# Optimization experiments

Hardware: AMD Instinct MI355X
Metric: run time of the kernel (lower is better)

## Reference

```python
import jax, jax.numpy as jnp
import numpy as np

N_NODES = 100000
N_EDGES = 1600000
IN_F = 256
OUT_F = 64
ALPHA = 0.2  # LeakyReLU negative slope


def setup_inputs() -> dict:
    key = jax.random.key(0)
    k1, k2, k3, k4 = jax.random.split(key, 4)
    x = jax.random.normal(k1, (N_NODES, IN_F), dtype=jnp.float32)
    indices = jax.random.randint(k2, (2, N_EDGES), 0, N_NODES, dtype=jnp.int64)
    # xavier_uniform with gain=1.414 ~ U(-b, b), b = gain*sqrt(6/(fan_in+fan_out))
    bW = 1.414 * np.sqrt(6.0 / (IN_F + OUT_F))
    W = jax.random.uniform(k3, (IN_F, OUT_F), dtype=jnp.float32, minval=-bW, maxval=bW)
    ba = 1.414 * np.sqrt(6.0 / (2 * OUT_F + 1))
    a = jax.random.uniform(k4, (2 * OUT_F, 1), dtype=jnp.float32, minval=-ba, maxval=ba)
    return {"x": x, "indices": indices, "W": W, "a": a}


def reference(x, indices, W, a):
    # h = X @ W  -> [N, F_out]
    h = x @ W
    N = h.shape[0]
    src = indices[0]  # segment ids (softmax rows / aggregation targets)
    dst = indices[1]  # gathered neighbor features

    # e_ij = leakyrelu([h_i || h_j] @ a) = leakyrelu(h_i@a1 + h_j@a2)
    # (identical math to concatenation, avoids materializing [E, 2F])
    a1 = a[:OUT_F, 0]
    a2 = a[OUT_F:, 0]
    s1 = h @ a1  # [N]
    s2 = h @ a2  # [N]
    logits = s1[src] + s2[dst]  # [E]
    e = jnp.where(logits > 0, logits, ALPHA * logits)

    # segment softmax over edges grouped by src (sp_softmax)
    m = jax.ops.segment_max(e, src, num_segments=N)
    ex = jnp.exp(e - m[src])
    denom = jax.ops.segment_sum(ex, src, num_segments=N)
    att = ex / denom[src]  # [E]

    # h_prime[i] = sum_j att_ij * h_j  (sp_matmul: weighted scatter-aggregate)
    h_prime = jax.ops.segment_sum(att[:, None] * h[dst], src, num_segments=N)

    # concat=True -> ELU
    return jax.nn.elu(h_prime)
```

## Files before the change

kernel.cpp:

```cpp
#include <hip/hip_runtime.h>
#include <hip/hip_bf16.h>
#include <math.h>

#define NN 100000
#define NE 1600000
#define INF_ 256
#define OF 64

#define NPB 128
#define NB  782
#define CAPB 2560
#define ED (CAPB + 128)
#define GEMMB 782
#define P1B 512
#define CH1 ((NE + P1B - 1) / P1B)
#define OVCAP 8192

constexpr float LRELU_ALPHA = 0.2f;

typedef __attribute__((ext_vector_type(8))) short short8;
typedef __attribute__((ext_vector_type(4))) float f32x4;

static __device__ __forceinline__ unsigned short f2bf(float f) {
    union { float f; unsigned int u; } v; v.f = f;
    unsigned int r = v.u + 0x7fff + ((v.u >> 16) & 1);
    return (unsigned short)(r >> 16);
}
static __device__ __forceinline__ float bf2f(unsigned short b) {
    union { unsigned int u; float f; } v; v.u = ((unsigned int)b) << 16;
    return v.f;
}
static __device__ __forceinline__ unsigned int pkbf(float a, float b) {
    union { __hip_bfloat162 h; unsigned int u; } c;
    c.h = __float22bfloat162_rn(make_float2(a, b));
    return c.u;
}

union S8 { short8 s; unsigned int u[4]; };

__global__ __launch_bounds__(256) void k_fused1(const float* __restrict__ x,
                                                const float* __restrict__ W,
                                                const float* __restrict__ a,
                                                const int* __restrict__ idx,
                                                int* __restrict__ cur_b,
                                                int* __restrict__ pairs,
                                                int2* __restrict__ ov_list,
                                                unsigned short* __restrict__ h,
                                                float* __restrict__ s1,
                                                float* __restrict__ s2) {
    __shared__ __align__(16) char smem[43008];
    int tid = threadIdx.x;

    if (blockIdx.x < GEMMB) {
        short* Wf  = (short*)smem;
        float* wal = (float*)(smem + 40960);

        {
            float t1 = 0.f, t2 = 0.f;
            const float* wr = W + tid * OF;
#pragma unroll 8
            for (int c = 0; c < OF; ++c) {
                float w = wr[c];
                t1 += w * a[c];
                t2 += w * a[OF + c];
            }
            wal[tid] = t1;
            wal[256 + tid] = t2;
        }
        __syncthreads();

        for (int i = tid; i < 2560; i += 256) {
            int ks = i / 320;
            int rem = i - ks * 320;
            int ct = rem >> 6;
            int l  = rem & 63;
            int kb = ks * 32 + ((l >> 4) << 3);
            int c  = l & 15;
            S8 v;
            if (ct < 4) {
                int col = ct * 16 + c;
#pragma unroll
                for (int j = 0; j < 4; ++j)
                    v.u[j] = pkbf(W[(size_t)(kb + 2 * j) * OF + col],
                                  W[(size_t)(kb + 2 * j + 1) * OF + col]);
            } else if (c < 2) {
                const float* src = wal + c * 256;
#pragma unroll
                for (int j = 0; j < 4; ++j)
                    v.u[j] = pkbf(src[kb + 2 * j], src[kb + 2 * j + 1]);
            } else {
#pragma unroll
                for (int j = 0; j < 4; ++j) v.u[j] = 0u;
            }
            ((short8*)Wf)[i] = v.s;
        }
        __syncthreads();

        int wid = tid >> 6, lane = tid & 63;
        int rowbase = blockIdx.x * 128 + wid * 32;
        int r0 = rowbase + (lane & 15);
        int koff = (lane >> 4) << 3;

        f32x4 acc[2][5];
#pragma unroll
        for (int rt = 0; rt < 2; ++rt)
#pragma unroll
            for (int ct = 0; ct < 5; ++ct) acc[rt][ct] = (f32x4){0.f, 0.f, 0.f, 0.f};

#pragma unroll 1
        for (int ks = 0; ks < 8; ++ks) {
            S8 af[2];
#pragma unroll
            for (int rt = 0; rt < 2; ++rt) {
                int r = r0 + rt * 16;
                if (r < NN) {
                    const float* p = x + (size_t)r * INF_ + ks * 32 + koff;
                    float4 xa = *(const float4*)p;
                    float4 xb = *(const float4*)(p + 4);
                    af[rt].u[0] = pkbf(xa.x, xa.y);
                    af[rt].u[1] = pkbf(xa.z, xa.w);
                    af[rt].u[2] = pkbf(xb.x, xb.y);
                    af[rt].u[3] = pkbf(xb.z, xb.w);
                } else {
#pragma unroll
                    for (int j = 0; j < 4; ++j) af[rt].u[j] = 0u;
                }
            }
#pragma unroll
            for (int rt = 0; rt < 2; ++rt)
#pragma unroll
                for (int ct = 0; ct < 5; ++ct)
                    acc[rt][ct] = __builtin_amdgcn_mfma_f32_16x16x32_bf16(
                        af[rt].s, ((short8*)Wf)[(ks * 5 + ct) * 64 + lane], acc[rt][ct], 0, 0, 0);
        }

        int c = lane & 15, rowq = lane >> 4;
#pragma unroll
        for (int rt = 0; rt < 2; ++rt) {
#pragma unroll
            for (int reg = 0; reg < 4; ++reg) {
                int r = rowbase + rt * 16 + rowq * 4 + reg;
                if (r < NN) {
#pragma unroll
                    for (int ct = 0; ct < 4; ++ct)
                        h[(size_t)r * OF + ct * 16 + c] = f2bf(acc[rt][ct][reg]);
                    float sv = acc[rt][4][reg];
                    if (c == 0)      s1[r] = sv;
                    else if (c == 1) s2[r] = sv;
                }
            }
        }
    } else {
        int blk = blockIdx.x - GEMMB;
        int* hist  = (int*)smem;
        int* gbase = (int*)smem + NB;
        for (int i = tid; i < NB; i += 256) hist[i] = 0;
        __syncthreads();
        int e0 = blk * CH1, e1 = min(e0 + CH1, NE);
        for (int e = e0 + tid; e < e1; e += 256)
            atomicAdd(&hist[idx[e] >> 7], 1);
        __syncthreads();
        for (int i = tid; i < NB; i += 256) {
            int c = hist[i];
            gbase[i] = c ? atomicAdd(&cur_b[i], c) : 0;
            hist[i] = 0;
        }
        __syncthreads();
        for (int e = e0 + tid; e < e1; e += 256) {
            int s = idx[e], d = idx[NE + e];
            int b = s >> 7;
            int p = gbase[b] + atomicAdd(&hist[b], 1);
            if (p < CAPB) pairs[b * CAPB + p] = ((s & 127) << 17) | d;
            else {
                int j = atomicAdd(&cur_b[NB], 1);
                if (j < OVCAP) ov_list[j] = make_int2(s, d);
            }
        }
    }
}

__global__ __launch_bounds__(256) void k_part2(const int* __restrict__ pairs,
                                               const int* __restrict__ cur_b,
                                               const int2* __restrict__ ov_list,
                                               const float* __restrict__ s1,
                                               const float* __restrict__ s2,
                                               int* __restrict__ start,
                                               int* __restrict__ deg,
                                               int2* __restrict__ el_g) {
    __shared__ int stage[ED];
    __shared__ int cnt[NPB], pfx[NPB], cur[NPB];
    __shared__ float s1l[NPB];
    __shared__ int extra;
    int tid = threadIdx.x, b = blockIdx.x;
    int node0 = b * NPB;

    if (tid < NPB) {
        cnt[tid] = 0;
        int g = node0 + tid;
        s1l[tid] = (g < NN) ? s1[g] : 0.f;
    }
    if (tid == 0) extra = 0;
    __syncthreads();

    int t_b = cur_b[b];
    int nin = min(t_b, CAPB);
    for (int i = tid; i < nin; i += 256) {
        int v = pairs[b * CAPB + i];
        stage[i] = v;
        atomicAdd(&cnt[v >> 17], 1);
    }
    if (t_b > CAPB) {
        int ovn = min(cur_b[NB], OVCAP);
        for (int i = tid; i < ovn; i += 256) {
            int2 e = ov_list[i];
            if ((e.x >> 7) == b) {
                int k = atomicAdd(&extra, 1);
                if (k < 128) {
                    stage[CAPB + k] = ((e.x & 127) << 17) | e.y;
                    atomicAdd(&cnt[e.x & 127], 1);
                }
            }
        }
    }
    __syncthreads();
    int ntot = nin + min(extra, 128);

    if (tid < NPB) pfx[tid] = cnt[tid];
    __syncthreads();
    for (int off = 1; off < NPB; off <<= 1) {
        int xv = (tid >= off && tid < NPB) ? pfx[tid - off] : 0;
        __syncthreads();
        if (tid < NPB) pfx[tid] += xv;
        __syncthreads();
    }
    if (tid < NPB) {
        int ex = pfx[tid] - cnt[tid];
        int g = node0 + tid;
        if (g < NN) { start[g] = b * CAPB + ex; deg[g] = cnt[tid]; }
        cur[tid] = ex;
    }
    __syncthreads();
    for (int i = tid; i < ntot; i += 256) {
        int v = stage[i];
        int ls = v >> 17, dst = v & 0x1FFFF;
        int p = atomicAdd(&cur[ls], 1);
        float lg = s1l[ls] + s2[dst];
        float elr = lg > 0.f ? lg : LRELU_ALPHA * lg;
        el_g[b * CAPB + p] = make_int2(dst, __float_as_int(expf(elr)));
    }
}

__global__ __launch_bounds__(256) void k_agg(const int2* __restrict__ el_g,
                                             const int* __restrict__ start,
                                             const int* __restrict__ deg,
                                             const unsigned short* __restrict__ h,
                                             float* __restrict__ out) {
    __shared__ int2 tile[4][64];
    int tid = threadIdx.x;
    int wid = tid >> 6, lane = tid & 63;
    int node = blockIdx.x * 4 + wid;
    if (node >= NN) return;

    int st = start[node];
    int dg = deg[node];
    int half = lane >> 5, f2 = lane & 31;
    float den = 0.f, ax = 0.f, ay = 0.f;

    for (int base = 0; base < dg; base += 64) {
        int cnt = min(64, dg - base);
        if (lane < cnt) {
            int2 pr = el_g[st + base + lane];
            den += __int_as_float(pr.y);
            tile[wid][lane] = pr;
        }
        asm volatile("s_waitcnt lgkmcnt(0)" ::: "memory");
#pragma unroll 4
        for (int j = half; j < cnt; j += 2) {
            int2 e = tile[wid][j];
            float ex = __int_as_float(e.y);
            unsigned int hv = *(const unsigned int*)(h + (size_t)e.x * OF + f2 * 2);
            ax += ex * bf2f((unsigned short)(hv & 0xFFFFu));
            ay += ex * bf2f((unsigned short)(hv >> 16));
        }
        asm volatile("" ::: "memory");
    }

#pragma unroll
    for (int off = 1; off < 64; off <<= 1) den += __shfl_xor(den, off, 64);
    ax += __shfl_xor(ax, 32, 64);
    ay += __shfl_xor(ay, 32, 64);

    float inv = den > 0.f ? 1.f / den : 0.f;
    float vx = ax * inv, vy = ay * inv;
    vx = vx > 0.f ? vx : expf(vx) - 1.f;
    vy = vy > 0.f ? vy : expf(vy) - 1.f;
    if (half == 0)
        *(float2*)(out + (size_t)node * OF + f2 * 2) = make_float2(vx, vy);
}

extern "C" void kernel_launch(void* const* d_in, const int* in_sizes, int n_in,
                              void* d_out, int out_size, void* d_ws, size_t ws_size,
                              hipStream_t stream) {
    const float* x   = (const float*)d_in[0];
    const int*   idx = (const int*)d_in[1];
    const float* W   = (const float*)d_in[2];
    const float* a   = (const float*)d_in[3];
    float* out = (float*)d_out;

    char* ws = (char*)d_ws;
    unsigned short* h = (unsigned short*)ws;  ws += sizeof(unsigned short) * (size_t)NN * OF;
    int*  pairs       = (int*)ws;             ws += sizeof(int) * (size_t)NB * CAPB;
    int2* el_g        = (int2*)ws;            ws += sizeof(int2) * (size_t)NB * CAPB;
    float* s1         = (float*)ws;           ws += sizeof(float) * NN;
    float* s2         = (float*)ws;           ws += sizeof(float) * NN;
    int*   start      = (int*)ws;             ws += sizeof(int) * NN;
    int*   deg        = (int*)ws;             ws += sizeof(int) * NN;
    int*   cur_b      = (int*)ws;             ws += sizeof(int) * (NB + 16);
    int2*  ov_list    = (int2*)ws;            ws += sizeof(int2) * OVCAP;

    hipMemsetAsync(cur_b, 0, sizeof(int) * (NB + 16), stream);
    k_fused1<<<GEMMB + P1B, 256, 0, stream>>>(x, W, a, idx, cur_b, pairs, ov_list, h, s1, s2);
    k_part2<<<NB, 256, 0, stream>>>(pairs, cur_b, ov_list, s1, s2, start, deg, el_g);
    k_agg<<<(NN + 3) / 4, 256, 0, stream>>>(el_g, start, deg, h, out);
}
```

Measured before the change: 289.0 us.

## Split fused GEMM/partition kernel and prefetch next x tile in GEMM

Breaks the fused kernel into three launches. A one-block prep kernel computes W@a once instead of in every GEMM block. A dedicated GEMM kernel with occupancy hint 4 register-prefetches the next K-slice of x while MFMAs run on the current one. The edge partition runs as its own kernel. This removes per-block redundant W@a work and hides x load latency, but gives up the overlap between GEMM and partition blocks and adds launch overhead.

```diff
diff --git a/kernel.cpp b/kernel.cpp
--- a/kernel.cpp
+++ b/kernel.cpp
@@ -38,143 +38,146 @@
 
 union S8 { short8 s; unsigned int u[4]; };
 
-__global__ __launch_bounds__(256) void k_fused1(const float* __restrict__ x,
-                                                const float* __restrict__ W,
-                                                const float* __restrict__ a,
-                                                const int* __restrict__ idx,
-                                                int* __restrict__ cur_b,
-                                                int* __restrict__ pairs,
-                                                int2* __restrict__ ov_list,
-                                                unsigned short* __restrict__ h,
-                                                float* __restrict__ s1,
-                                                float* __restrict__ s2) {
-    __shared__ __align__(16) char smem[43008];
+__global__ __launch_bounds__(256) void k_prep(const float* __restrict__ W,
+                                              const float* __restrict__ a,
+                                              float* __restrict__ wa) {
+    int r = threadIdx.x;
+    float t1 = 0.f, t2 = 0.f;
+#pragma unroll 8
+    for (int c = 0; c < OF; ++c) {
+        float w = W[r * OF + c];
+        t1 += w * a[c];
+        t2 += w * a[OF + c];
+    }
+    wa[r] = t1;
+    wa[256 + r] = t2;
+}
+
+__global__ __launch_bounds__(256, 4) void k_gemm(const float* __restrict__ x,
+                                                 const float* __restrict__ W,
+                                                 const float* __restrict__ wa,
+                                                 unsigned short* __restrict__ h,
+                                                 float* __restrict__ s1,
+                                                 float* __restrict__ s2) {
+    __shared__ short Wf[2560 * 8];
     int tid = threadIdx.x;
-
-    if (blockIdx.x < GEMMB) {
-        short* Wf  = (short*)smem;
-        float* wal = (float*)(smem + 40960);
-
-        {
-            float t1 = 0.f, t2 = 0.f;
-            const float* wr = W + tid * OF;
-#pragma unroll 8
-            for (int c = 0; c < OF; ++c) {
-                float w = wr[c];
-                t1 += w * a[c];
-                t2 += w * a[OF + c];
+    for (int i = tid; i < 2560; i += 256) {
+        int ks = i / 320;
+        int rem = i - ks * 320;
+        int ct = rem >> 6;
+        int l  = rem & 63;
+        int kb = ks * 32 + ((l >> 4) << 3);
+        int c  = l & 15;
+        S8 v;
+        if (ct < 4) {
+            int col = ct * 16 + c;
+#pragma unroll
+            for (int j = 0; j < 4; ++j)
+                v.u[j] = pkbf(W[(size_t)(kb + 2 * j) * OF + col],
+                              W[(size_t)(kb + 2 * j + 1) * OF + col]);
+        } else if (c < 2) {
+            const float* src = wa + c * 256;
+#pragma unroll
+            for (int j = 0; j < 4; ++j)
+                v.u[j] = pkbf(src[kb + 2 * j], src[kb + 2 * j + 1]);
+        } else {
+#pragma unroll
+            for (int j = 0; j < 4; ++j) v.u[j] = 0u;
+        }
+        ((short8*)Wf)[i] = v.s;
+    }
+    __syncthreads();
+
+    int wid = tid >> 6, lane = tid & 63;
+    int rowbase = blockIdx.x * 128 + wid * 32;
+    int r0 = rowbase + (lane & 15);
+    int koff = (lane >> 4) << 3;
+    bool ok0 = (r0 < NN), ok1 = (r0 + 16 < NN);
+    const float* p0 = x + (size_t)r0 * INF_ + koff;
+    const float* p1 = p0 + (size_t)16 * INF_;
+
+    f32x4 acc[2][5];
+#pragma unroll
+    for (int rt = 0; rt < 2; ++rt)
+#pragma unroll
+        for (int ct = 0; ct < 5; ++ct) acc[rt][ct] = (f32x4){0.f, 0.f, 0.f, 0.f};
+
+    float4 ca0, cb0, ca1, cb1;
+    float4 na0, nb0, na1, nb1;
+    ca0 = ok0 ? *(const float4*)p0 : make_float4(0, 0, 0, 0);
+    cb0 = ok0 ? *(const float4*)(p0 + 4) : make_float4(0, 0, 0, 0);
+    ca1 = ok1 ? *(const float4*)p1 : make_float4(0, 0, 0, 0);
+    cb1 = ok1 ? *(const float4*)(p1 + 4) : make_float4(0, 0, 0, 0);
+
+#pragma unroll 1
+    for (int ks = 0; ks < 8; ++ks) {
+        if (ks < 7) {
+            const float* q0 = p0 + (ks + 1) * 32;
+            const float* q1 = p1 + (ks + 1) * 32;
+            na0 = ok0 ? *(const float4*)q0 : make_float4(0, 0, 0, 0);
+            nb0 = ok0 ? *(const float4*)(q0 + 4) : make_float4(0, 0, 0, 0);
+            na1 = ok1 ? *(const float4*)q1 : make_float4(0, 0, 0, 0);
+            nb1 = ok1 ? *(const float4*)(q1 + 4) : make_float4(0, 0, 0, 0);
+        }
+        S8 af[2];
+        af[0].u[0] = pkbf(ca0.x, ca0.y); af[0].u[1] = pkbf(ca0.z, ca0.w);
+        af[0].u[2] = pkbf(cb0.x, cb0.y); af[0].u[3] = pkbf(cb0.z, cb0.w);
+        af[1].u[0] = pkbf(ca1.x, ca1.y); af[1].u[1] = pkbf(ca1.z, ca1.w);
+        af[1].u[2] = pkbf(cb1.x, cb1.y); af[1].u[3] = pkbf(cb1.z, cb1.w);
+#pragma unroll
+        for (int rt = 0; rt < 2; ++rt)
+#pragma unroll
+            for (int ct = 0; ct < 5; ++ct)
+                acc[rt][ct] = __builtin_amdgcn_mfma_f32_16x16x32_bf16(
+                    af[rt].s, ((short8*)Wf)[(ks * 5 + ct) * 64 + lane], acc[rt][ct], 0, 0, 0);
+        ca0 = na0; cb0 = nb0; ca1 = na1; cb1 = nb1;
+    }
+
+    int c = lane & 15, rowq = lane >> 4;
+#pragma unroll
+    for (int rt = 0; rt < 2; ++rt) {
+#pragma unroll
+        for (int reg = 0; reg < 4; ++reg) {
+            int r = rowbase + rt * 16 + rowq * 4 + reg;
+            if (r < NN) {
+#pragma unroll
+                for (int ct = 0; ct < 4; ++ct)
+                    h[(size_t)r * OF + ct * 16 + c] = f2bf(acc[rt][ct][reg]);
+                float sv = acc[rt][4][reg];
+                if (c == 0)      s1[r] = sv;
+                else if (c == 1) s2[r] = sv;
             }
-            wal[tid] = t1;
-            wal[256 + tid] = t2;
-        }
-        __syncthreads();
-
-        for (int i = tid; i < 2560; i += 256) {
-            int ks = i / 320;
-            int rem = i - ks * 320;
-            int ct = rem >> 6;
-            int l  = rem & 63;
-            int kb = ks * 32 + ((l >> 4) << 3);
-            int c  = l & 15;
-            S8 v;
-            if (ct < 4) {
-                int col = ct * 16 + c;
-#pragma unroll
-                for (int j = 0; j < 4; ++j)
-                    v.u[j] = pkbf(W[(size_t)(kb + 2 * j) * OF + col],
-                                  W[(size_t)(kb + 2 * j + 1) * OF + col]);
-            } else if (c < 2) {
-                const float* src = wal + c * 256;
-#pragma unroll
-                for (int j = 0; j < 4; ++j)
-                    v.u[j] = pkbf(src[kb + 2 * j], src[kb + 2 * j + 1]);
-            } else {
-#pragma unroll
-                for (int j = 0; j < 4; ++j) v.u[j] = 0u;
-            }
-            ((short8*)Wf)[i] = v.s;
-        }
-        __syncthreads();
-
-        int wid = tid >> 6, lane = tid & 63;
-        int rowbase = blockIdx.x * 128 + wid * 32;
-        int r0 = rowbase + (lane & 15);
-        int koff = (lane >> 4) << 3;
-
-        f32x4 acc[2][5];
-#pragma unroll
-        for (int rt = 0; rt < 2; ++rt)
-#pragma unroll
-            for (int ct = 0; ct < 5; ++ct) acc[rt][ct] = (f32x4){0.f, 0.f, 0.f, 0.f};
-
-#pragma unroll 1
-        for (int ks = 0; ks < 8; ++ks) {
-            S8 af[2];
-#pragma unroll
-            for (int rt = 0; rt < 2; ++rt) {
-                int r = r0 + rt * 16;
-                if (r < NN) {
-                    const float* p = x + (size_t)r * INF_ + ks * 32 + koff;
-                    float4 xa = *(const float4*)p;
-                    float4 xb = *(const float4*)(p + 4);
-                    af[rt].u[0] = pkbf(xa.x, xa.y);
-                    af[rt].u[1] = pkbf(xa.z, xa.w);
-                    af[rt].u[2] = pkbf(xb.x, xb.y);
-                    af[rt].u[3] = pkbf(xb.z, xb.w);
-                } else {
-#pragma unroll
-                    for (int j = 0; j < 4; ++j) af[rt].u[j] = 0u;
-                }
-            }
-#pragma unroll
-            for (int rt = 0; rt < 2; ++rt)
-#pragma unroll
-                for (int ct = 0; ct < 5; ++ct)
-                    acc[rt][ct] = __builtin_amdgcn_mfma_f32_16x16x32_bf16(
-                        af[rt].s, ((short8*)Wf)[(ks * 5 + ct) * 64 + lane], acc[rt][ct], 0, 0, 0);
-        }
-
-        int c = lane & 15, rowq = lane >> 4;
-#pragma unroll
-        for (int rt = 0; rt < 2; ++rt) {
-#pragma unroll
-            for (int reg = 0; reg < 4; ++reg) {
-                int r = rowbase + rt * 16 + rowq * 4 + reg;
-                if (r < NN) {
-#pragma unroll
-                    for (int ct = 0; ct < 4; ++ct)
-                        h[(size_t)r * OF + ct * 16 + c] = f2bf(acc[rt][ct][reg]);
-                    float sv = acc[rt][4][reg];
-                    if (c == 0)      s1[r] = sv;
-                    else if (c == 1) s2[r] = sv;
-                }
-            }
-        }
-    } else {
-        int blk = blockIdx.x - GEMMB;
-        int* hist  = (int*)smem;
-        int* gbase = (int*)smem + NB;
-        for (int i = tid; i < NB; i += 256) hist[i] = 0;
-        __syncthreads();
-        int e0 = blk * CH1, e1 = min(e0 + CH1, NE);
-        for (int e = e0 + tid; e < e1; e += 256)
-            atomicAdd(&hist[idx[e] >> 7], 1);
-        __syncthreads();
-        for (int i = tid; i < NB; i += 256) {
-            int c = hist[i];
-            gbase[i] = c ? atomicAdd(&cur_b[i], c) : 0;
-            hist[i] = 0;
-        }
-        __syncthreads();
-        for (int e = e0 + tid; e < e1; e += 256) {
-            int s = idx[e], d = idx[NE + e];
-            int b = s >> 7;
-            int p = gbase[b] + atomicAdd(&hist[b], 1);
-            if (p < CAPB) pairs[b * CAPB + p] = ((s & 127) << 17) | d;
-            else {
-                int j = atomicAdd(&cur_b[NB], 1);
-                if (j < OVCAP) ov_list[j] = make_int2(s, d);
-            }
+        }
+    }
+}
+
+__global__ __launch_bounds__(256) void k_part1(const int* __restrict__ idx,
+                                               int* __restrict__ cur_b,
+                                               int* __restrict__ pairs,
+                                               int2* __restrict__ ov_list) {
+    __shared__ int hist[NB];
+    __shared__ int gbase[NB];
+    int tid = threadIdx.x, blk = blockIdx.x;
+    for (int i = tid; i < NB; i += 256) hist[i] = 0;
+    __syncthreads();
+    int e0 = blk * CH1, e1 = min(e0 + CH1, NE);
+    for (int e = e0 + tid; e < e1; e += 256)
+        atomicAdd(&hist[idx[e] >> 7], 1);
+    __syncthreads();
+    for (int i = tid; i < NB; i += 256) {
+        int c = hist[i];
+        gbase[i] = c ? atomicAdd(&cur_b[i], c) : 0;
+        hist[i] = 0;
+    }
+    __syncthreads();
+    for (int e = e0 + tid; e < e1; e += 256) {
+        int s = idx[e], d = idx[NE + e];
+        int b = s >> 7;
+        int p = gbase[b] + atomicAdd(&hist[b], 1);
+        if (p < CAPB) pairs[b * CAPB + p] = ((s & 127) << 17) | d;
+        else {
+            int j = atomicAdd(&cur_b[NB], 1);
+            if (j < OVCAP) ov_list[j] = make_int2(s, d);
         }
     }
 }
@@ -317,9 +320,12 @@
     int*   deg        = (int*)ws;             ws += sizeof(int) * NN;
     int*   cur_b      = (int*)ws;             ws += sizeof(int) * (NB + 16);
     int2*  ov_list    = (int2*)ws;            ws += sizeof(int2) * OVCAP;
+    float* wa         = (float*)ws;           ws += sizeof(float) * 512;
 
     hipMemsetAsync(cur_b, 0, sizeof(int) * (NB + 16), stream);
-    k_fused1<<<GEMMB + P1B, 256, 0, stream>>>(x, W, a, idx, cur_b, pairs, ov_list, h, s1, s2);
+    k_prep<<<1, 256, 0, stream>>>(W, a, wa);
+    k_gemm<<<GEMMB, 256, 0, stream>>>(x, W, wa, h, s1, s2);
+    k_part1<<<P1B, 256, 0, stream>>>(idx, cur_b, pairs, ov_list);
     k_part2<<<NB, 256, 0, stream>>>(pairs, cur_b, ov_list, s1, s2, start, deg, el_g);
     k_agg<<<(NN + 3) / 4, 256, 0, stream>>>(el_g, start, deg, h, out);
 }
```

Result: slower. 296.3 us (+2.5%).

## Hoist W·a precompute into prep kernel and keep score fragment in registers

Applied to the files above, without the earlier changes.

Moves the per-block W·a reduction into a tiny separate kernel, so each GEMM block no longer recomputes it. The fifth MFMA column tile (attention scores) is held in per-lane registers instead of shared memory, which cuts LDS from 43 KB to 32 KB and adds launch bounds of 3 blocks per CU. The K loop is fully unrolled, and the row-bounds branches are replaced with clamped addresses so x loads can issue early. In exchange it adds an extra kernel launch and more register pressure, which could collide with the occupancy target.

```diff
diff --git a/kernel.cpp b/kernel.cpp
--- a/kernel.cpp
+++ b/kernel.cpp
@@ -38,103 +38,109 @@
 
 union S8 { short8 s; unsigned int u[4]; };
 
-__global__ __launch_bounds__(256) void k_fused1(const float* __restrict__ x,
-                                                const float* __restrict__ W,
-                                                const float* __restrict__ a,
-                                                const int* __restrict__ idx,
-                                                int* __restrict__ cur_b,
-                                                int* __restrict__ pairs,
-                                                int2* __restrict__ ov_list,
-                                                unsigned short* __restrict__ h,
-                                                float* __restrict__ s1,
-                                                float* __restrict__ s2) {
-    __shared__ __align__(16) char smem[43008];
+__global__ __launch_bounds__(256) void k_prep(const float* __restrict__ W,
+                                              const float* __restrict__ a,
+                                              float* __restrict__ wa) {
+    int r = threadIdx.x;
+    float t1 = 0.f, t2 = 0.f;
+#pragma unroll 8
+    for (int c = 0; c < OF; ++c) {
+        float w = W[r * OF + c];
+        t1 += w * a[c];
+        t2 += w * a[OF + c];
+    }
+    wa[r] = t1;
+    wa[256 + r] = t2;
+}
+
+__global__ __launch_bounds__(256, 3) void k_fused1(const float* __restrict__ x,
+                                                   const float* __restrict__ W,
+                                                   const float* __restrict__ wa,
+                                                   const int* __restrict__ idx,
+                                                   int* __restrict__ cur_b,
+                                                   int* __restrict__ pairs,
+                                                   int2* __restrict__ ov_list,
+                                                   unsigned short* __restrict__ h,
+                                                   float* __restrict__ s1,
+                                                   float* __restrict__ s2) {
+    __shared__ __align__(16) char smem[32768];
     int tid = threadIdx.x;
 
     if (blockIdx.x < GEMMB) {
-        short* Wf  = (short*)smem;
-        float* wal = (float*)(smem + 40960);
-
-        {
-            float t1 = 0.f, t2 = 0.f;
-            const float* wr = W + tid * OF;
-#pragma unroll 8
-            for (int c = 0; c < OF; ++c) {
-                float w = wr[c];
-                t1 += w * a[c];
-                t2 += w * a[OF + c];
-            }
-            wal[tid] = t1;
-            wal[256 + tid] = t2;
-        }
-        __syncthreads();
-
-        for (int i = tid; i < 2560; i += 256) {
-            int ks = i / 320;
-            int rem = i - ks * 320;
-            int ct = rem >> 6;
-            int l  = rem & 63;
+        short* Wf = (short*)smem;
+        for (int i = tid; i < 2048; i += 256) {
+            int ks = i >> 8;
+            int ct = (i >> 6) & 3;
+            int l  = i & 63;
             int kb = ks * 32 + ((l >> 4) << 3);
-            int c  = l & 15;
+            int col = ct * 16 + (l & 15);
             S8 v;
-            if (ct < 4) {
-                int col = ct * 16 + c;
-#pragma unroll
-                for (int j = 0; j < 4; ++j)
-                    v.u[j] = pkbf(W[(size_t)(kb + 2 * j) * OF + col],
-                                  W[(size_t)(kb + 2 * j + 1) * OF + col]);
-            } else if (c < 2) {
-                const float* src = wal + c * 256;
-#pragma unroll
-                for (int j = 0; j < 4; ++j)
-                    v.u[j] = pkbf(src[kb + 2 * j], src[kb + 2 * j + 1]);
-            } else {
-#pragma unroll
-                for (int j = 0; j < 4; ++j) v.u[j] = 0u;
-            }
+#pragma unroll
+            for (int j = 0; j < 4; ++j)
+                v.u[j] = pkbf(W[(size_t)(kb + 2 * j) * OF + col],
+                              W[(size_t)(kb + 2 * j + 1) * OF + col]);
             ((short8*)Wf)[i] = v.s;
         }
-        __syncthreads();
 
         int wid = tid >> 6, lane = tid & 63;
         int rowbase = blockIdx.x * 128 + wid * 32;
-        int r0 = rowbase + (lane & 15);
+        int c = lane & 15;
         int koff = (lane >> 4) << 3;
 
+        short8 frag5[8];
+        {
+#pragma unroll
+            for (int ks = 0; ks < 8; ++ks) {
+                S8 v;
+                if (c < 2) {
+                    const float* src = wa + c * 256 + ks * 32 + koff;
+                    float4 u0 = *(const float4*)src;
+                    float4 u1 = *(const float4*)(src + 4);
+                    v.u[0] = pkbf(u0.x, u0.y); v.u[1] = pkbf(u0.z, u0.w);
+                    v.u[2] = pkbf(u1.x, u1.y); v.u[3] = pkbf(u1.z, u1.w);
+                } else {
+                    v.u[0] = 0u; v.u[1] = 0u; v.u[2] = 0u; v.u[3] = 0u;
+                }
+                frag5[ks] = v.s;
+            }
+        }
+        __syncthreads();
+
+        int r0 = rowbase + c;
+        int rc0 = min(r0, NN - 1);
+        int rc1 = min(r0 + 16, NN - 1);
+        const float* p0 = x + (size_t)rc0 * INF_ + koff;
+        const float* p1 = x + (size_t)rc1 * INF_ + koff;
+
         f32x4 acc[2][5];
 #pragma unroll
         for (int rt = 0; rt < 2; ++rt)
 #pragma unroll
             for (int ct = 0; ct < 5; ++ct) acc[rt][ct] = (f32x4){0.f, 0.f, 0.f, 0.f};
 
-#pragma unroll 1
+#pragma unroll
         for (int ks = 0; ks < 8; ++ks) {
+            float4 xa0 = *(const float4*)(p0 + ks * 32);
+            float4 xb0 = *(const float4*)(p0 + ks * 32 + 4);
+            float4 xa1 = *(const float4*)(p1 + ks * 32);
+            float4 xb1 = *(const float4*)(p1 + ks * 32 + 4);
             S8 af[2];
+            af[0].u[0] = pkbf(xa0.x, xa0.y); af[0].u[1] = pkbf(xa0.z, xa0.w);
+            af[0].u[2] = pkbf(xb0.x, xb0.y); af[0].u[3] = pkbf(xb0.z, xb0.w);
+            af[1].u[0] = pkbf(xa1.x, xa1.y); af[1].u[1] = pkbf(xa1.z, xa1.w);
+            af[1].u[2] = pkbf(xb1.x, xb1.y); af[1].u[3] = pkbf(xb1.z, xb1.w);
 #pragma unroll
             for (int rt = 0; rt < 2; ++rt) {
-                int r = r0 + rt * 16;
-                if (r < NN) {
-                    const float* p = x + (size_t)r * INF_ + ks * 32 + koff;
-                    float4 xa = *(const float4*)p;
-                    float4 xb = *(const float4*)(p + 4);
-                    af[rt].u[0] = pkbf(xa.x, xa.y);
-                    af[rt].u[1] = pkbf(xa.z, xa.w);
-                    af[rt].u[2] = pkbf(xb.x, xb.y);
-                    af[rt].u[3] = pkbf(xb.z, xb.w);
-                } else {
-#pragma unroll
-                    for (int j = 0; j < 4; ++j) af[rt].u[j] = 0u;
-                }
-            }
-#pragma unroll
-            for (int rt = 0; rt < 2; ++rt)
-#pragma unroll
-                for (int ct = 0; ct < 5; ++ct)
+#pragma unroll
+                for (int ct = 0; ct < 4; ++ct)
                     acc[rt][ct] = __builtin_amdgcn_mfma_f32_16x16x32_bf16(
-                        af[rt].s, ((short8*)Wf)[(ks * 5 + ct) * 64 + lane], acc[rt][ct], 0, 0, 0);
-        }
-
-        int c = lane & 15, rowq = lane >> 4;
+                        af[rt].s, ((short8*)Wf)[(ks * 4 + ct) * 64 + lane], acc[rt][ct], 0, 0, 0);
+                acc[rt][4] = __builtin_amdgcn_mfma_f32_16x16x32_bf16(
+                    af[rt].s, frag5[ks], acc[rt][4], 0, 0, 0);
+            }
+        }
+
+        int rowq = lane >> 4;
 #pragma unroll
         for (int rt = 0; rt < 2; ++rt) {
 #pragma unroll
@@ -161,8 +167,8 @@
             atomicAdd(&hist[idx[e] >> 7], 1);
         __syncthreads();
         for (int i = tid; i < NB; i += 256) {
-            int c = hist[i];
-            gbase[i] = c ? atomicAdd(&cur_b[i], c) : 0;
+            int cc = hist[i];
+            gbase[i] = cc ? atomicAdd(&cur_b[i], cc) : 0;
             hist[i] = 0;
         }
         __syncthreads();
@@ -317,9 +323,11 @@
     int*   deg        = (int*)ws;             ws += sizeof(int) * NN;
     int*   cur_b      = (int*)ws;             ws += sizeof(int) * (NB + 16);
     int2*  ov_list    = (int2*)ws;            ws += sizeof(int2) * OVCAP;
+    float* wa         = (float*)ws;           ws += sizeof(float) * 512;
 
     hipMemsetAsync(cur_b, 0, sizeof(int) * (NB + 16), stream);
-    k_fused1<<<GEMMB + P1B, 256, 0, stream>>>(x, W, a, idx, cur_b, pairs, ov_list, h, s1, s2);
+    k_prep<<<1, 256, 0, stream>>>(W, a, wa);
+    k_fused1<<<GEMMB + P1B, 256, 0, stream>>>(x, W, wa, idx, cur_b, pairs, ov_list, h, s1, s2);
     k_part2<<<NB, 256, 0, stream>>>(pairs, cur_b, ov_list, s1, s2, start, deg, el_g);
     k_agg<<<(NN + 3) / 4, 256, 0, stream>>>(el_g, start, deg, h, out);
 }
```

Measured after the change: 288.8 us. No clear change (-0.1%).
